# Kernel optimization log

Hardware: AMD Instinct MI355X
Metric: run time of the kernel (lower is better)

The kernel has to match this reference:

```python
import jax, jax.numpy as jnp
import numpy as np

# Module hyperparameters (from init_kwargs)
KERNEL = (16, 16)     # sliding window shape; Linear in_features = prod = 256
STRIDE = (8, 8)       # window stride
DILATION = (4, 4)     # per-window output tile; Linear out_features = prod = 16
# padding = 0, bias = False (module defaults)


def setup_inputs() -> dict:
    key = jax.random.key(0)
    k1, k2 = jax.random.split(key)
    x = jax.random.normal(k1, (32, 1024, 1024), dtype=jnp.float32)
    # torch nn.Linear weight convention: [out_features, in_features] = [16, 256]
    weight = jax.random.normal(k2, (16, 256), dtype=jnp.float32) / 16.0  # ~1/sqrt(in)
    return {"x": x, "weight": weight}


def reference(x, weight):
    # im2col: extract all sliding windows, flattened in (kh, kw) row-major order
    # (matches torch's window.flatten() since there is a single implicit channel).
    B = x.shape[0]
    patches = jax.lax.conv_general_dilated_patches(
        x[:, None],                 # [B, 1, H, W]
        filter_shape=KERNEL,
        window_strides=STRIDE,
        padding='VALID',
    )                               # [B, prod(KERNEL)=256, nH=127, nW=127]
    nH, nW = patches.shape[2], patches.shape[3]
    d0, d1 = DILATION
    # Dense per-patch linear: y = W @ flat_window   (bias=False)
    out = jnp.einsum('bkij,ok->bijo', patches, weight)   # [B, nH, nW, 16]
    # Each patch's 16 outputs reshape to a (4,4) tile placed at its output site.
    out = out.reshape(B, nH, nW, d0, d1)
    out = out.transpose(0, 1, 3, 2, 4).reshape(B, nH * d0, nW * d1)  # [B, 508, 508]
    return out
```

## Files before the change

kernel.cpp:

```cpp
#include <hip/hip_runtime.h>
#include <hip/hip_bf16.h>


typedef __attribute__((ext_vector_type(8))) short short8;
typedef __attribute__((ext_vector_type(4))) float f32x4;

__device__ __forceinline__ unsigned pkrn(float a, float b) {
    __hip_bfloat162 h = __float22bfloat162_rn(make_float2(a, b));
    unsigned r;
    __builtin_memcpy(&r, &h, 4);
    return r;
}

__device__ __forceinline__ short8 cvt8(float4 v0, float4 v1) {
    uint4 u = make_uint4(pkrn(v0.x, v0.y), pkrn(v0.z, v0.w),
                         pkrn(v1.x, v1.y), pkrn(v1.z, v1.w));
    return __builtin_bit_cast(short8, u);
}

__global__ __launch_bounds__(256, 4)
void conv_ring(const float* __restrict__ x,
               const float* __restrict__ w,
               float* __restrict__ out) {
    const int tid  = threadIdx.x;
    const int lane = tid & 63;
    const int wv   = tid >> 6;
    const int bx   = blockIdx.x;
    const int jt   = bx & 7;
    const int it   = bx >> 3;
    const int b    = blockIdx.y;

    const float* xb = x + (size_t)b * (1024 * 1024);

    const int m  = lane & 15;
    const int kb = (lane >> 4) & 1;
    const int hi = lane >> 5;
    const int p  = lane >> 4;

    short8 wfrag[8];
    #pragma unroll
    for (int s = 0; s < 8; ++s) {
        const float* wp = w + m * 256 + s * 32 + (lane >> 4) * 8;
        wfrag[s] = cvt8(*(const float4*)wp, *(const float4*)(wp + 4));
    }

    int colf = jt * 128 + m * 8 + kb * 8;
    if (colf > 1016) colf = 1016;
    const int jp    = jt * 16 + m;
    const int iband = it * 16 + wv * 4;

#define ISSUE(B, k) do {                                                     \
        const int _t = (k) >> 2, _q = (k) & 3;                               \
        int _r0 = (iband + _t) * 8; if (_r0 > 1008) _r0 = 1008;              \
        const float* _p0 = xb + (size_t)(_r0 + hi + 4 * _q) * 1024 + colf;   \
        B[0] = *(const float4*)_p0;          B[1] = *(const float4*)(_p0 + 4);        \
        B[2] = *(const float4*)(_p0 + 2048); B[3] = *(const float4*)(_p0 + 2048 + 4); \
    } while (0)

#define COMP(B, k) do {                                                      \
        const int _q = (k) & 3;                                              \
        acc = __builtin_amdgcn_mfma_f32_16x16x32_bf16(                       \
                  wfrag[2 * _q],     cvt8(B[0], B[1]), acc, 0, 0, 0);        \
        acc = __builtin_amdgcn_mfma_f32_16x16x32_bf16(                       \
                  wfrag[2 * _q + 1], cvt8(B[2], B[3]), acc, 0, 0, 0);        \
    } while (0)

#define STORE(t) do {                                                        \
        const int _ip = iband + (t);                                         \
        if (_ip < 127 && jp < 127) {                                         \
            float* _op = out + (size_t)b * (508 * 508)                       \
                             + (_ip * 4 + p) * 508 + jp * 4;                 \
            *(float4*)_op = *(float4*)&acc;                                  \
        }                                                                    \
        acc = (f32x4){0.f, 0.f, 0.f, 0.f};                                   \
    } while (0)

    float4 Q0[4], Q1[4], Q2[4], Q3[4];
    f32x4 acc = {0.f, 0.f, 0.f, 0.f};

    ISSUE(Q0, 0); ISSUE(Q1, 1); ISSUE(Q2, 2);

    COMP(Q0, 0);   ISSUE(Q3, 3);
    COMP(Q1, 1);   ISSUE(Q0, 4);
    COMP(Q2, 2);   ISSUE(Q1, 5);
    COMP(Q3, 3);   ISSUE(Q2, 6);   STORE(0);
    COMP(Q0, 4);   ISSUE(Q3, 7);
    COMP(Q1, 5);   ISSUE(Q0, 8);
    COMP(Q2, 6);   ISSUE(Q1, 9);
    COMP(Q3, 7);   ISSUE(Q2, 10);  STORE(1);
    COMP(Q0, 8);   ISSUE(Q3, 11);
    COMP(Q1, 9);   ISSUE(Q0, 12);
    COMP(Q2, 10);  ISSUE(Q1, 13);
    COMP(Q3, 11);  ISSUE(Q2, 14);  STORE(2);
    COMP(Q0, 12);  ISSUE(Q3, 15);
    COMP(Q1, 13);
    COMP(Q2, 14);
    COMP(Q3, 15);  STORE(3);

#undef ISSUE
#undef COMP
#undef STORE
}

extern "C" void kernel_launch(void* const* d_in, const int* in_sizes, int n_in,
                              void* d_out, int out_size, void* d_ws, size_t ws_size,
                              hipStream_t stream) {
    const float* x = (const float*)d_in[0];
    const float* w = (const float*)d_in[1];
    float* out = (float*)d_out;
    dim3 grid(64, 32);
    conv_ring<<<grid, dim3(256, 1, 1), 0, stream>>>(x, w, out);
}
```

Baseline: 42.78 us.

## Make blocks persist over four column tiles with cross-tile load prefetch

Each block now handles four consecutive column tiles in a loop instead of one, and the grid shrinks from 2048 to 512 blocks. The last three issues of each tile prefetch the first loads of the next tile, so the register ring pipeline runs across tile boundaries and the per-block prologue and weight-fragment load are paid less often. Launch bounds drop to two blocks per SIMD-occupancy hint, which allows more registers but lowers occupancy. Fewer blocks (512 on a large GPU) may also leave CUs underused, and the final iteration issues redundant prefetches.

After: 40.85 us. 1.05x faster.

```diff
diff --git a/kernel.cpp b/kernel.cpp
--- a/kernel.cpp
+++ b/kernel.cpp
@@ -18,24 +18,26 @@
     return __builtin_bit_cast(short8, u);
 }
 
-__global__ __launch_bounds__(256, 4)
-void conv_ring(const float* __restrict__ x,
-               const float* __restrict__ w,
-               float* __restrict__ out) {
+__global__ __launch_bounds__(256, 2)
+void conv_persist(const float* __restrict__ x,
+                  const float* __restrict__ w,
+                  float* __restrict__ out) {
     const int tid  = threadIdx.x;
     const int lane = tid & 63;
     const int wv   = tid >> 6;
-    const int bx   = blockIdx.x;
-    const int jt   = bx & 7;
-    const int it   = bx >> 3;
-    const int b    = blockIdx.y;
+    const int band = blockIdx.x >> 1;
+    const int half = blockIdx.x & 1;
+    const int b    = band >> 3;
+    const int it   = band & 7;
 
     const float* xb = x + (size_t)b * (1024 * 1024);
+    float* ob = out + (size_t)b * (508 * 508);
 
     const int m  = lane & 15;
     const int kb = (lane >> 4) & 1;
     const int hi = lane >> 5;
     const int p  = lane >> 4;
+    const int iband = it * 16 + wv * 4;
 
     short8 wfrag[8];
     #pragma unroll
@@ -44,15 +46,12 @@
         wfrag[s] = cvt8(*(const float4*)wp, *(const float4*)(wp + 4));
     }
 
-    int colf = jt * 128 + m * 8 + kb * 8;
-    if (colf > 1016) colf = 1016;
-    const int jp    = jt * 16 + m;
-    const int iband = it * 16 + wv * 4;
+#define COLF(jt) ({ int _c = (jt) * 128 + m * 8 + kb * 8; if (_c > 1016) _c = 1016; _c; })
 
-#define ISSUE(B, k) do {                                                     \
+#define ISSUE(B, k, jt) do {                                                 \
         const int _t = (k) >> 2, _q = (k) & 3;                               \
         int _r0 = (iband + _t) * 8; if (_r0 > 1008) _r0 = 1008;              \
-        const float* _p0 = xb + (size_t)(_r0 + hi + 4 * _q) * 1024 + colf;   \
+        const float* _p0 = xb + (size_t)(_r0 + hi + 4 * _q) * 1024 + COLF(jt); \
         B[0] = *(const float4*)_p0;          B[1] = *(const float4*)(_p0 + 4);        \
         B[2] = *(const float4*)(_p0 + 2048); B[3] = *(const float4*)(_p0 + 2048 + 4); \
     } while (0)
@@ -65,11 +64,11 @@
                   wfrag[2 * _q + 1], cvt8(B[2], B[3]), acc, 0, 0, 0);        \
     } while (0)
 
-#define STORE(t) do {                                                        \
+#define STORE(t, jt) do {                                                    \
         const int _ip = iband + (t);                                         \
-        if (_ip < 127 && jp < 127) {                                         \
-            float* _op = out + (size_t)b * (508 * 508)                       \
-                             + (_ip * 4 + p) * 508 + jp * 4;                 \
+        const int _jp = (jt) * 16 + m;                                       \
+        if (_ip < 127 && _jp < 127) {                                        \
+            float* _op = ob + (_ip * 4 + p) * 508 + _jp * 4;                 \
             *(float4*)_op = *(float4*)&acc;                                  \
         }                                                                    \
         acc = (f32x4){0.f, 0.f, 0.f, 0.f};                                   \
@@ -78,25 +77,36 @@
     float4 Q0[4], Q1[4], Q2[4], Q3[4];
     f32x4 acc = {0.f, 0.f, 0.f, 0.f};
 
-    ISSUE(Q0, 0); ISSUE(Q1, 1); ISSUE(Q2, 2);
+    {
+        const int jt0 = half * 4;
+        ISSUE(Q0, 0, jt0); ISSUE(Q1, 1, jt0); ISSUE(Q2, 2, jt0);
+    }
 
-    COMP(Q0, 0);   ISSUE(Q3, 3);
-    COMP(Q1, 1);   ISSUE(Q0, 4);
-    COMP(Q2, 2);   ISSUE(Q1, 5);
-    COMP(Q3, 3);   ISSUE(Q2, 6);   STORE(0);
-    COMP(Q0, 4);   ISSUE(Q3, 7);
-    COMP(Q1, 5);   ISSUE(Q0, 8);
-    COMP(Q2, 6);   ISSUE(Q1, 9);
-    COMP(Q3, 7);   ISSUE(Q2, 10);  STORE(1);
-    COMP(Q0, 8);   ISSUE(Q3, 11);
-    COMP(Q1, 9);   ISSUE(Q0, 12);
-    COMP(Q2, 10);  ISSUE(Q1, 13);
-    COMP(Q3, 11);  ISSUE(Q2, 14);  STORE(2);
-    COMP(Q0, 12);  ISSUE(Q3, 15);
-    COMP(Q1, 13);
-    COMP(Q2, 14);
-    COMP(Q3, 15);  STORE(3);
+    #pragma unroll
+    for (int s = 0; s < 4; ++s) {
+        const int jt = half * 4 + s;
+        const int sn = (s < 3) ? s + 1 : 3;
+        const int jn = half * 4 + sn;
 
+        COMP(Q0, 0);   ISSUE(Q3, 3,  jt);
+        COMP(Q1, 1);   ISSUE(Q0, 4,  jt);
+        COMP(Q2, 2);   ISSUE(Q1, 5,  jt);
+        COMP(Q3, 3);   ISSUE(Q2, 6,  jt);  STORE(0, jt);
+        COMP(Q0, 4);   ISSUE(Q3, 7,  jt);
+        COMP(Q1, 5);   ISSUE(Q0, 8,  jt);
+        COMP(Q2, 6);   ISSUE(Q1, 9,  jt);
+        COMP(Q3, 7);   ISSUE(Q2, 10, jt);  STORE(1, jt);
+        COMP(Q0, 8);   ISSUE(Q3, 11, jt);
+        COMP(Q1, 9);   ISSUE(Q0, 12, jt);
+        COMP(Q2, 10);  ISSUE(Q1, 13, jt);
+        COMP(Q3, 11);  ISSUE(Q2, 14, jt);  STORE(2, jt);
+        COMP(Q0, 12);  ISSUE(Q3, 15, jt);
+        COMP(Q1, 13);  ISSUE(Q0, 0,  jn);
+        COMP(Q2, 14);  ISSUE(Q1, 1,  jn);
+        COMP(Q3, 15);  ISSUE(Q2, 2,  jn);  STORE(3, jt);
+    }
+
+#undef COLF
 #undef ISSUE
 #undef COMP
 #undef STORE
@@ -108,6 +118,5 @@
     const float* x = (const float*)d_in[0];
     const float* w = (const float*)d_in[1];
     float* out = (float*)d_out;
-    dim3 grid(64, 32);
-    conv_ring<<<grid, dim3(256, 1, 1), 0, stream>>>(x, w, out);
+    conv_persist<<<dim3(512, 1, 1), dim3(256, 1, 1), 0, stream>>>(x, w, out);
 }
```
